# Optimization experiments

Hardware: AMD Instinct MI355X
Metric: run time of the kernel (lower is better)

## Reference

```python
import jax, jax.numpy as jnp
import numpy as np

H = 16   # num_heads
D = 16   # key_dim == output_dim (required by the module's reshape)
F = 64   # input feature dim


def setup_inputs() -> dict:
    key = jax.random.key(0)
    ks = jax.random.split(key, 8)
    B, N, Kn = 4, 4096, 32
    scale = 1.0 / np.sqrt(F)
    return {
        "inp": jax.random.normal(ks[0], (B, N, Kn, F), dtype=jnp.float32),
        "query": jax.random.normal(ks[1], (B, N, F), dtype=jnp.float32),
        "Wq": jax.random.normal(ks[2], (F, H * D), dtype=jnp.float32) * scale,
        "bq": jnp.zeros((H * D,), dtype=jnp.float32),
        "Wk": jax.random.normal(ks[3], (F, H * D), dtype=jnp.float32) * scale,
        "bk": jnp.zeros((H * D,), dtype=jnp.float32),
        "Wv": jax.random.normal(ks[4], (F, H * D), dtype=jnp.float32) * scale,
        "bv": jnp.zeros((H * D,), dtype=jnp.float32),
    }


def reference(inp, query, Wq, bq, Wk, bk, Wv, bv):
    B, N, Kn, _ = inp.shape
    # Dense projections
    Q = query @ Wq + bq                    # [B, N, H*D]
    K = inp @ Wk + bk                      # [B, N, Kn, H*D]
    V = inp @ Wv + bv                      # [B, N, Kn, H*D]
    # Faithful reshape (plain reshape of last dims, as in the TF code)
    Q = Q.reshape(B, N, H, 1, D)           # query broadcast axis of size 1
    K = K.reshape(B, N, H, Kn, D)
    V = V.reshape(B, N, H, Kn, D)
    # scaled dot-product attention per point over its Kn neighbors
    w = jnp.einsum('bnhqd,bnhkd->bnhqk', Q, K) / jnp.sqrt(jnp.float32(D))
    w = jax.nn.softmax(w, axis=-1)         # [B, N, H, 1, Kn]
    out = jnp.einsum('bnhqk,bnhkd->bnhqd', w, V)  # [B, N, H, 1, D]
    return out.reshape(B, N, H * D)
```

## Files before the change

### kernel.cpp

```cpp
#include <hip/hip_runtime.h>

#define KN 32
#define FF 64
#define CC 256
#define KSTRB 264
#define VSTB 40
#define VTOFFB (KN * KSTRB)
#define NITER 16
#define QSTRIDE 264
#define WSTRIDE 36


typedef __attribute__((ext_vector_type(8)))  short bf16x8;
typedef __attribute__((ext_vector_type(16))) float f32x16;
typedef __attribute__((ext_vector_type(4)))  float f32x4;

__device__ inline unsigned short f2bf(float f) {
    union { float f; unsigned u; } v; v.f = f;
    unsigned u = v.u + 0x7fffu + ((v.u >> 16) & 1u);
    return (unsigned short)(u >> 16);
}
__device__ inline unsigned cvt_pk_bf16(float a, float b) {
    unsigned r;
    asm("v_cvt_pk_bf16_f32 %0, %1, %2" : "=v"(r) : "v"(a), "v"(b));
    return r;
}
__device__ inline bf16x8 pack8(float4 a, float4 b) {
    union { bf16x8 v; unsigned u[4]; } r;
    r.u[0] = cvt_pk_bf16(a.x, a.y);  r.u[1] = cvt_pk_bf16(a.z, a.w);
    r.u[2] = cvt_pk_bf16(b.x, b.y);  r.u[3] = cvt_pk_bf16(b.z, b.w);
    return r.v;
}
__device__ inline float bflo(unsigned u) { return __uint_as_float(u << 16); }
__device__ inline float bfhi(unsigned u) { return __uint_as_float(u & 0xffff0000u); }

__device__ inline void lds_barrier() {
    asm volatile("s_waitcnt lgkmcnt(0)" ::: "memory");
    __builtin_amdgcn_s_barrier();
}

__global__ __launch_bounds__(256, 2)
void attn_one(const float* __restrict__ inp,
              const float* __restrict__ query,
              const float* __restrict__ Wq,
              const float* __restrict__ bq,
              const float* __restrict__ Wk,
              const float* __restrict__ bk,
              const float* __restrict__ Wv,
              const float* __restrict__ bv,
              float* __restrict__ out, int nPoints)
{
    __shared__ __align__(16) unsigned short kvS[KN * KSTRB + CC * VSTB];
    __shared__ unsigned short qAllS[NITER * QSTRIDE];
    __shared__ float wS[16 * WSTRIDE];

    const int tid  = threadIdx.x;
    const int wave = tid >> 6;
    const int L    = tid & 63;
    const int Lm   = L & 31;
    const int Lh   = L >> 5;
    const int h    = tid >> 4;
    const int d    = tid & 15;
    const int bid  = blockIdx.x;
    const int grid = gridDim.x;

    float* qIn = (float*)kvS;
    {
        const int i  = tid >> 4;
        const int f4 = (tid & 15) * 4;
        const int p  = bid + i * grid;
        if (p < nPoints)
            *(float4*)(qIn + i * 68 + f4) =
                *(const float4*)(query + (size_t)p * FF + f4);
    }

    float4 pf[8];
    {
        const float* arow = inp + (size_t)bid * (KN * FF) + Lm * FF + Lh * 8;
#pragma unroll
        for (int s = 0; s < 4; ++s) {
            pf[2 * s]     = *(const float4*)(arow + s * 16);
            pf[2 * s + 1] = *(const float4*)(arow + s * 16 + 4);
        }
    }

    bf16x8 Bf[4][4];
#pragma unroll
    for (int t = 0; t < 4; ++t) {
        const float* W  = (t < 2) ? Wk : Wv;
        const int ch    = (2 * wave + (t & 1)) * 32 + Lm;
#pragma unroll
        for (int s = 0; s < 4; ++s) {
            union { bf16x8 v; unsigned u[4]; } r;
#pragma unroll
            for (int jj = 0; jj < 4; ++jj) {
                const int f = s * 16 + Lh * 8 + 2 * jj;
                r.u[jj] = cvt_pk_bf16(W[(size_t)f * CC + ch], W[(size_t)(f + 1) * CC + ch]);
            }
            Bf[t][s] = r.v;
        }
    }
    float biasV[2];
    biasV[0] = bv[(2 * wave + 0) * 32 + Lm];
    biasV[1] = bv[(2 * wave + 1) * 32 + Lm];
    float4 bkK[2][4];
#pragma unroll
    for (int t = 0; t < 2; ++t)
#pragma unroll
        for (int g = 0; g < 4; ++g)
            bkK[t][g] = *(const float4*)(bk + (2 * wave + t) * 32 + 8 * g + 4 * Lh);

    const int nq = L & 15;
    const int kq = (L >> 4) * 8;
    bf16x8 Bq[4][2];
    float  bqv[4];
#pragma unroll
    for (int tt = 0; tt < 4; ++tt) {
        const int ch = wave * 64 + tt * 16 + nq;
        bqv[tt] = bq[ch];
#pragma unroll
        for (int s = 0; s < 2; ++s) {
            union { bf16x8 v; unsigned u[4]; } r;
#pragma unroll
            for (int jj = 0; jj < 4; ++jj) {
                const int f = s * 32 + kq + 2 * jj;
                r.u[jj] = cvt_pk_bf16(Wq[(size_t)f * CC + ch], Wq[(size_t)(f + 1) * CC + ch]);
            }
            Bq[tt][s] = r.v;
        }
    }

    __syncthreads();

    {
        bf16x8 Aq[2];
        const int im = L & 15;
#pragma unroll
        for (int s = 0; s < 2; ++s) {
            const float* qr = qIn + im * 68 + s * 32 + kq;
            Aq[s] = pack8(*(const float4*)qr, *(const float4*)(qr + 4));
        }
#pragma unroll
        for (int tt = 0; tt < 4; ++tt) {
            f32x4 qa = {bqv[tt], bqv[tt], bqv[tt], bqv[tt]};
#pragma unroll
            for (int s = 0; s < 2; ++s)
                qa = __builtin_amdgcn_mfma_f32_16x16x32_bf16(Aq[s], Bq[tt][s], qa, 0, 0, 0);
            const int ch = wave * 64 + tt * 16 + nq;
#pragma unroll
            for (int r = 0; r < 4; ++r) {
                const int ip = (L >> 4) * 4 + r;
                qAllS[ip * QSTRIDE + ch] = f2bf(qa[r] * 0.25f);
            }
        }
    }
    __syncthreads();

    const int sR  = d & 7;
    const int j0  = 2 * h + (d >> 3);
    const int vb0 = VTOFFB + 40 * d + 2 * h;

    for (int it = 0, p = bid; p < nPoints; ++it, p += grid) {
        bf16x8 Af[4];
#pragma unroll
        for (int s = 0; s < 4; ++s) Af[s] = pack8(pf[2 * s], pf[2 * s + 1]);

        const int pn = p + grid;
        if (pn < nPoints) {
            const float* arow = inp + (size_t)pn * (KN * FF) + Lm * FF + Lh * 8;
#pragma unroll
            for (int s = 0; s < 4; ++s) {
                pf[2 * s]     = *(const float4*)(arow + s * 16);
                pf[2 * s + 1] = *(const float4*)(arow + s * 16 + 4);
            }
        }

        f32x16 acc[4];
#pragma unroll
        for (int t = 0; t < 2; ++t)
#pragma unroll
            for (int g = 0; g < 4; ++g)
#pragma unroll
                for (int e = 0; e < 4; ++e) acc[t][4 * g + e] = bkK[t][g][e];
#pragma unroll
        for (int t = 2; t < 4; ++t)
#pragma unroll
            for (int r = 0; r < 16; ++r) acc[t][r] = biasV[t - 2];

        __builtin_amdgcn_s_setprio(1);
#pragma unroll
        for (int s = 0; s < 4; ++s) {
#pragma unroll
            for (int t = 0; t < 2; ++t)
                acc[t] = __builtin_amdgcn_mfma_f32_32x32x16_bf16(Bf[t][s], Af[s], acc[t], 0, 0, 0);
#pragma unroll
            for (int t = 2; t < 4; ++t)
                acc[t] = __builtin_amdgcn_mfma_f32_32x32x16_bf16(Af[s], Bf[t][s], acc[t], 0, 0, 0);
        }
        __builtin_amdgcn_s_setprio(0);

#pragma unroll
        for (int t = 0; t < 2; ++t) {
            unsigned short* kr = kvS + Lm * KSTRB + (2 * wave + t) * 32 + 4 * Lh;
#pragma unroll
            for (int g = 0; g < 4; ++g) {
                const unsigned p0 = cvt_pk_bf16(acc[t][4 * g],     acc[t][4 * g + 1]);
                const unsigned p1 = cvt_pk_bf16(acc[t][4 * g + 2], acc[t][4 * g + 3]);
                *(uint2*)(kr + 8 * g) = make_uint2(p0, p1);
            }
        }
#pragma unroll
        for (int t = 2; t < 4; ++t) {
            const int col = (2 * wave + (t & 1)) * 32 + Lm;
            unsigned short* vr = kvS + VTOFFB + col * VSTB + 4 * Lh;
#pragma unroll
            for (int g = 0; g < 4; ++g) {
                const unsigned p0 = cvt_pk_bf16(acc[t][4 * g],     acc[t][4 * g + 1]);
                const unsigned p1 = cvt_pk_bf16(acc[t][4 * g + 2], acc[t][4 * g + 3]);
                *(uint2*)(vr + 8 * g) = make_uint2(p0, p1);
            }
        }

        const unsigned short* qp = qAllS + it * QSTRIDE + h * 16;
        uint4 qA = *(const uint4*)qp;
        uint4 qB = *(const uint4*)(qp + 8);

        lds_barrier();

        const unsigned short* kb = kvS + j0 * KSTRB + sR * 32;
        union { uint4 v; unsigned u[4]; } ckb[4];
#pragma unroll
        for (int w = 0; w < 4; ++w)
            ckb[w].v = *(const uint4*)(kb + 8 * w);

        union { uint4 v; unsigned u[4]; } ua, ub;
        ua.v = qA;  ub.v = qB;
        float qv[16];
#pragma unroll
        for (int j = 0; j < 4; ++j) {
            qv[2 * j]         = bflo(ua.u[j]);
            qv[2 * j + 1]     = bfhi(ua.u[j]);
            qv[8 + 2 * j]     = bflo(ub.u[j]);
            qv[8 + 2 * j + 1] = bfhi(ub.u[j]);
        }

        float l0a = 0.f, l0b = 0.f, l1a = 0.f, l1b = 0.f;
#pragma unroll
        for (int dd = 0; dd < 8; ++dd) {
            const unsigned u0 = ckb[dd >> 2].u[dd & 3];
            const unsigned u1 = ckb[2 + (dd >> 2)].u[dd & 3];
            l0a = fmaf(qv[2 * dd],     bflo(u0), l0a);
            l0b = fmaf(qv[2 * dd + 1], bfhi(u0), l0b);
            l1a = fmaf(qv[2 * dd],     bflo(u1), l1a);
            l1b = fmaf(qv[2 * dd + 1], bfhi(u1), l1b);
        }
        const float l0 = l0a + l0b;
        const float l1 = l1a + l1b;

        float m = fmaxf(l0, l1);
        m = fmaxf(m, __shfl_xor(m, 1));
        m = fmaxf(m, __shfl_xor(m, 2));
        m = fmaxf(m, __shfl_xor(m, 4));
        m = fmaxf(m, __shfl_xor(m, 8));
        float e0 = __expf(l0 - m), e1 = __expf(l1 - m);
        float s2 = e0 + e1;
        s2 += __shfl_xor(s2, 1);
        s2 += __shfl_xor(s2, 2);
        s2 += __shfl_xor(s2, 4);
        s2 += __shfl_xor(s2, 8);
        const float inv = 1.0f / s2;
        *(float2*)(wS + h * WSTRIDE + 2 * d) = make_float2(e0 * inv, e1 * inv);
        __builtin_amdgcn_wave_barrier();

        float4 wv[8];
#pragma unroll
        for (int g = 0; g < 8; ++g)
            wv[g] = *(const float4*)(wS + h * WSTRIDE + 4 * g);

        float o0 = 0.f, o1 = 0.f, o2 = 0.f, o3 = 0.f;
#pragma unroll
        for (int mI = 0; mI < 16; mI += 2) {
            const unsigned va = *(const unsigned*)(kvS + vb0 + 640 * mI);
            const unsigned vb = *(const unsigned*)(kvS + vb0 + 640 * (mI + 1));
            o0 = fmaf(wv[mI >> 2][mI & 3],                   bflo(va), o0);
            o1 = fmaf(wv[4 + (mI >> 2)][mI & 3],             bfhi(va), o1);
            o2 = fmaf(wv[(mI + 1) >> 2][(mI + 1) & 3],       bflo(vb), o2);
            o3 = fmaf(wv[4 + ((mI + 1) >> 2)][(mI + 1) & 3], bfhi(vb), o3);
        }
        out[(size_t)p * CC + tid] = (o0 + o1) + (o2 + o3);

        lds_barrier();
    }
}

extern "C" void kernel_launch(void* const* d_in, const int* in_sizes, int n_in,
                              void* d_out, int out_size, void* d_ws, size_t ws_size,
                              hipStream_t stream) {
    const float* inp   = (const float*)d_in[0];
    const float* query = (const float*)d_in[1];
    const float* Wq    = (const float*)d_in[2];
    const float* bq    = (const float*)d_in[3];
    const float* Wk    = (const float*)d_in[4];
    const float* bk    = (const float*)d_in[5];
    const float* Wv    = (const float*)d_in[6];
    const float* bv    = (const float*)d_in[7];
    float* out = (float*)d_out;

    const int nPoints = in_sizes[0] / (KN * FF);
    const int grid    = (nPoints + NITER - 1) / NITER;

    attn_one<<<grid, 256, 0, stream>>>(inp, query, Wq, bq, Wk, bk, Wv, bv,
                                       out, nPoints);
}
```

Baseline: 254.4 us.

## Double-buffer K/V shared memory to overlap next projection with attention

Splits the K/V LDS staging area into two halves and software-pipelines the loop so the MFMA projection for the next point is written into the alternate buffer while the current point's softmax and weighted sum read the other. This removes one block barrier per iteration and lets matrix work overlap with scalar attention work. The V row stride also shrinks from 40 to 36 elements, which changes the LDS bank mapping and keeps the doubled buffer smaller. In exchange, LDS usage roughly doubles for that region, which may limit occupancy below the two-blocks-per-CU target.

```diff
diff --git a/kernel.cpp b/kernel.cpp
--- a/kernel.cpp
+++ b/kernel.cpp
@@ -4,8 +4,9 @@
 #define FF 64
 #define CC 256
 #define KSTRB 264
-#define VSTB 40
+#define VSTB 36
 #define VTOFFB (KN * KSTRB)
+#define HALFB (KN * KSTRB + CC * VSTB)
 #define NITER 16
 #define QSTRIDE 264
 #define WSTRIDE 36
@@ -50,7 +51,7 @@
               const float* __restrict__ bv,
               float* __restrict__ out, int nPoints)
 {
-    __shared__ __align__(16) unsigned short kvS[KN * KSTRB + CC * VSTB];
+    __shared__ __align__(16) unsigned short kvS[2 * HALFB];
     __shared__ unsigned short qAllS[NITER * QSTRIDE];
     __shared__ float wS[16 * WSTRIDE];
 
@@ -156,25 +157,7 @@
     }
     __syncthreads();
 
-    const int sR  = d & 7;
-    const int j0  = 2 * h + (d >> 3);
-    const int vb0 = VTOFFB + 40 * d + 2 * h;
-
-    for (int it = 0, p = bid; p < nPoints; ++it, p += grid) {
-        bf16x8 Af[4];
-#pragma unroll
-        for (int s = 0; s < 4; ++s) Af[s] = pack8(pf[2 * s], pf[2 * s + 1]);
-
-        const int pn = p + grid;
-        if (pn < nPoints) {
-            const float* arow = inp + (size_t)pn * (KN * FF) + Lm * FF + Lh * 8;
-#pragma unroll
-            for (int s = 0; s < 4; ++s) {
-                pf[2 * s]     = *(const float4*)(arow + s * 16);
-                pf[2 * s + 1] = *(const float4*)(arow + s * 16 + 4);
-            }
-        }
-
+    auto project = [&](unsigned short* __restrict__ bp, const bf16x8 (&Af)[4]) {
         f32x16 acc[4];
 #pragma unroll
         for (int t = 0; t < 2; ++t)
@@ -201,7 +184,7 @@
 
 #pragma unroll
         for (int t = 0; t < 2; ++t) {
-            unsigned short* kr = kvS + Lm * KSTRB + (2 * wave + t) * 32 + 4 * Lh;
+            unsigned short* kr = bp + Lm * KSTRB + (2 * wave + t) * 32 + 4 * Lh;
 #pragma unroll
             for (int g = 0; g < 4; ++g) {
                 const unsigned p0 = cvt_pk_bf16(acc[t][4 * g],     acc[t][4 * g + 1]);
@@ -212,7 +195,7 @@
 #pragma unroll
         for (int t = 2; t < 4; ++t) {
             const int col = (2 * wave + (t & 1)) * 32 + Lm;
-            unsigned short* vr = kvS + VTOFFB + col * VSTB + 4 * Lh;
+            unsigned short* vr = bp + VTOFFB + col * VSTB + 4 * Lh;
 #pragma unroll
             for (int g = 0; g < 4; ++g) {
                 const unsigned p0 = cvt_pk_bf16(acc[t][4 * g],     acc[t][4 * g + 1]);
@@ -220,14 +203,40 @@
                 *(uint2*)(vr + 8 * g) = make_uint2(p0, p1);
             }
         }
-
-        const unsigned short* qp = qAllS + it * QSTRIDE + h * 16;
-        uint4 qA = *(const uint4*)qp;
-        uint4 qB = *(const uint4*)(qp + 8);
-
-        lds_barrier();
-
-        const unsigned short* kb = kvS + j0 * KSTRB + sR * 32;
+    };
+
+    {
+        bf16x8 Af[4];
+#pragma unroll
+        for (int s = 0; s < 4; ++s) Af[s] = pack8(pf[2 * s], pf[2 * s + 1]);
+
+        const int p1 = bid + grid;
+        if (p1 < nPoints) {
+            const float* arow = inp + (size_t)p1 * (KN * FF) + Lm * FF + Lh * 8;
+#pragma unroll
+            for (int s = 0; s < 4; ++s) {
+                pf[2 * s]     = *(const float4*)(arow + s * 16);
+                pf[2 * s + 1] = *(const float4*)(arow + s * 16 + 4);
+            }
+        }
+        project(kvS, Af);
+    }
+    uint4 qA = *(const uint4*)(qAllS + h * 16);
+    uint4 qB = *(const uint4*)(qAllS + h * 16 + 8);
+
+    lds_barrier();
+
+    const int sR = d & 7;
+    const int j0 = 2 * h + (d >> 3);
+
+    int cur = 0;
+    for (int it = 0, p = bid; p < nPoints; ++it, p += grid) {
+        const unsigned short* bc = kvS + cur * HALFB;
+        unsigned short* bn       = kvS + (cur ^ 1) * HALFB;
+        const int  pn   = p + grid;
+        const bool have = (pn < nPoints);
+
+        const unsigned short* kb = bc + j0 * KSTRB + sR * 32;
         union { uint4 v; unsigned u[4]; } ckb[4];
 #pragma unroll
         for (int w = 0; w < 4; ++w)
@@ -277,19 +286,41 @@
         for (int g = 0; g < 8; ++g)
             wv[g] = *(const float4*)(wS + h * WSTRIDE + 4 * g);
 
+        const unsigned short* vb = bc + VTOFFB + VSTB * d + 2 * h;
         float o0 = 0.f, o1 = 0.f, o2 = 0.f, o3 = 0.f;
 #pragma unroll
         for (int mI = 0; mI < 16; mI += 2) {
-            const unsigned va = *(const unsigned*)(kvS + vb0 + 640 * mI);
-            const unsigned vb = *(const unsigned*)(kvS + vb0 + 640 * (mI + 1));
+            const unsigned va = *(const unsigned*)(vb + 16 * VSTB * mI);
+            const unsigned vx = *(const unsigned*)(vb + 16 * VSTB * (mI + 1));
             o0 = fmaf(wv[mI >> 2][mI & 3],                   bflo(va), o0);
             o1 = fmaf(wv[4 + (mI >> 2)][mI & 3],             bfhi(va), o1);
-            o2 = fmaf(wv[(mI + 1) >> 2][(mI + 1) & 3],       bflo(vb), o2);
-            o3 = fmaf(wv[4 + ((mI + 1) >> 2)][(mI + 1) & 3], bfhi(vb), o3);
+            o2 = fmaf(wv[(mI + 1) >> 2][(mI + 1) & 3],       bflo(vx), o2);
+            o3 = fmaf(wv[4 + ((mI + 1) >> 2)][(mI + 1) & 3], bfhi(vx), o3);
         }
         out[(size_t)p * CC + tid] = (o0 + o1) + (o2 + o3);
 
+        if (have) {
+            bf16x8 Af[4];
+#pragma unroll
+            for (int s = 0; s < 4; ++s) Af[s] = pack8(pf[2 * s], pf[2 * s + 1]);
+
+            const int pn2 = pn + grid;
+            if (pn2 < nPoints) {
+                const float* arow = inp + (size_t)pn2 * (KN * FF) + Lm * FF + Lh * 8;
+#pragma unroll
+                for (int s = 0; s < 4; ++s) {
+                    pf[2 * s]     = *(const float4*)(arow + s * 16);
+                    pf[2 * s + 1] = *(const float4*)(arow + s * 16 + 4);
+                }
+            }
+            project(bn, Af);
+
+            qA = *(const uint4*)(qAllS + (it + 1) * QSTRIDE + h * 16);
+            qB = *(const uint4*)(qAllS + (it + 1) * QSTRIDE + h * 16 + 8);
+        }
+
         lds_barrier();
+        cur ^= 1;
     }
 }
 
```

After: 280.9 us. +10.4%, slower.
